# Performance work log

Hardware: AMD Instinct MI355X
Metric: run time of the kernel (lower is better)

## Reference

```python
import jax, jax.numpy as jnp
import numpy as np

B, FEAT, HID, LAT, NQ, NEMB = 2048, 840, 256, 128, 12, 512


def setup_inputs() -> dict:
    key = jax.random.key(0)
    ks = jax.random.split(key, 6)
    return {
        "x": jax.random.normal(ks[0], (B, FEAT), jnp.float32),
        "w1": jax.random.normal(ks[1], (HID, 1, 3), jnp.float32) * 0.1,   # Conv1d(1->256, k=3)
        "b1": jnp.zeros((HID,), jnp.float32),
        "w2": jax.random.normal(ks[2], (LAT, HID, 3), jnp.float32) * 0.05,  # Conv1d(256->128, k=3)
        "b2": jnp.zeros((LAT,), jnp.float32),
        # 12 codebooks of (512, 128), init uniform(-1/n_emb, 1/n_emb) per the torch code
        "codebooks": jax.random.uniform(ks[3], (NQ, NEMB, LAT), jnp.float32, -1.0 / NEMB, 1.0 / NEMB),
    }


def _encode(x, w1, b1, w2, b2):
    # x: (B, FEAT) -> unsqueeze channel dim -> NCW conv stack -> adaptive avg pool(1)
    h = x[:, None, :]  # (B, 1, FEAT)
    h = jax.lax.conv_general_dilated(h, w1, (1,), 'SAME',
                                     dimension_numbers=('NCH', 'OIH', 'NCH'))
    h = jax.nn.relu(h + b1[None, :, None])
    h = jax.lax.conv_general_dilated(h, w2, (1,), 'SAME',
                                     dimension_numbers=('NCH', 'OIH', 'NCH'))
    h = jax.nn.relu(h + b2[None, :, None])
    return h.mean(axis=2)  # AdaptiveAvgPool1d(1) + squeeze -> (B, LAT)


def _rvq(z_flat, codebooks):
    # sequential residual VQ: 12 stages of cdist -> argmin -> gather -> residual update
    def step(residual, cb):
        # squared L2 distances: ||r||^2 - 2 r C^T + ||c||^2, shape (B, NEMB)
        d = (jnp.sum(residual ** 2, axis=1, keepdims=True)
             - 2.0 * (residual @ cb.T)
             + jnp.sum(cb ** 2, axis=1)[None, :])
        idx = jnp.argmin(d, axis=1)          # (B,)
        q = cb[idx]                          # (B, LAT) embedding gather
        residual = residual - jax.lax.stop_gradient(q)  # .detach() in torch
        return residual, (q, idx)

    _, (qs, idxs) = jax.lax.scan(step, z_flat, codebooks)  # qs: (NQ, B, LAT)
    return qs.sum(axis=0), idxs.T  # (B, LAT), (B, NQ)


def reference(x, w1, b1, w2, b2, codebooks):
    z = _encode(x, w1, b1, w2, b2)            # (B, LAT)
    zq, idx = _rvq(z, codebooks)              # L = 1 so flat == (B, LAT)
    return zq[:, None, :], idx[:, None, :]    # (B, 1, LAT), (B, 1, NQ)
```

## Files before the change

kernel.cpp:

```cpp
#include <hip/hip_runtime.h>

#define B_SZ 2048
#define FEAT 840
#define HID  256
#define LAT  128
#define NQ   12
#define NEMB 512

#define T_SUB 40
#define NTILE 21
#define HSTR  46
#define H2STR 21
#define CQ    64
#define HBUF  (CQ * HSTR)

#define W2R_FLOATS ((size_t)HID * 384)
#define CBN_FLOATS ((size_t)NQ * NEMB)

__device__ __forceinline__ float np8_combine(const float* r) {
    float sA = __fadd_rn(r[0], r[1]);
    float sB = __fadd_rn(r[2], r[3]);
    float sC = __fadd_rn(r[4], r[5]);
    float sD = __fadd_rn(r[6], r[7]);
    return __fadd_rn(__fadd_rn(sA, sB), __fadd_rn(sC, sD));
}

__global__ __launch_bounds__(256) void w2r_kernel(const float* __restrict__ w2,
                                                  float* __restrict__ w2r)
{
    int p = blockIdx.x * 256 + threadIdx.x;
    if (p >= HID * 384) return;
    int c2 = p / 384, r = p - c2 * 384;
    int ly = r / 6, jk = r - ly * 6;
    int j = jk / 3, k = jk - j * 3;
    w2r[p] = w2[(size_t)(ly*2 + j)*768 + c2*3 + k];
}

__global__ __launch_bounds__(256) void cbn_kernel(const float* __restrict__ cb,
                                                  float* __restrict__ cbn)
{
    int p = blockIdx.x * 256 + threadIdx.x;
    if (p >= NQ * NEMB) return;
    const float* __restrict__ cp = cb + (size_t)p * LAT;
    float c8[8];
#pragma unroll
    for (int j = 0; j < 8; ++j) {
        float c = cp[j];
        c8[j] = __fmul_rn(c, c);
    }
    for (int i = 8; i < LAT; i += 8)
#pragma unroll
        for (int j = 0; j < 8; ++j) {
            float c = cp[i+j];
            c8[j] = __fadd_rn(c8[j], __fmul_rn(c, c));
        }
    cbn[p] = np8_combine(c8);
}

template <int USE_WR>
__global__ __launch_bounds__(256) void enc_kernel(
    const float* __restrict__ x,  const float* __restrict__ w1,
    const float* __restrict__ b1, const float* __restrict__ w2,
    const float* __restrict__ w2r,
    const float* __restrict__ b2, float* __restrict__ zout)
{
    __shared__ float xp[FEAT + 4];
    __shared__ float h1s[HBUF];
    __shared__ float leafs[LAT * 8];

    const int tid = threadIdx.x;
    const int b   = blockIdx.x;
    const int tx  = tid & 3;
    const int ly  = tid >> 2;
    const int u0  = tx * 10;

    const int ach   = tid >> 2;
    const int piece = tid & 3;
    const int tpb   = piece * 11;
    const int tpe   = (piece == 3) ? 42 : tpb + 11;

    float b2v[2];
    b2v[0] = b2[ly*2 + 0];
    b2v[1] = b2[ly*2 + 1];

    for (int i = tid; i < FEAT + 2; i += 256)
        xp[i] = (i >= 1 && i <= FEAT) ? x[(size_t)b*FEAT + i - 1] : 0.f;

    float racc[8];
    int leaf_id = 0, leaf_pos = 0;
#pragma unroll
    for (int j = 0; j < 8; ++j) racc[j] = 0.f;

    __syncthreads();
    for (int t0 = 0; t0 < FEAT; t0 += T_SUB) {
        const bool edge = (t0 == 0) | (t0 + T_SUB == FEAT);

        float sk[2][10][3];
#pragma unroll
        for (int j = 0; j < 2; ++j)
#pragma unroll
            for (int i = 0; i < 10; ++i)
#pragma unroll
                for (int k = 0; k < 3; ++k) sk[j][i][k] = 0.f;

#pragma unroll 1
        for (int qf = 0; qf < 4; ++qf) {
            {
                const int c = qf*CQ + ach;
                const float wA = w1[c*3+0], wB = w1[c*3+1], wC = w1[c*3+2];
                const float bb = b1[c];
                if (edge) {
                    for (int tp = tpb; tp < tpe; ++tp) {
                        int tg = t0 - 1 + tp;
                        float v = 0.f;
                        if (tg >= 0 && tg < FEAT) {
                            float s = __fadd_rn(__fadd_rn(__fmul_rn(wA, xp[tg]),
                                                          __fmul_rn(wB, xp[tg+1])),
                                                __fmul_rn(wC, xp[tg+2]));
                            s = __fadd_rn(s, bb);
                            v = s > 0.f ? s : 0.f;
                        }
                        h1s[ach*HSTR + tp] = v;
                    }
                } else {
#pragma unroll 11
                    for (int tp = tpb; tp < tpe; ++tp) {
                        int tg = t0 - 1 + tp;
                        float s = __fadd_rn(__fadd_rn(__fmul_rn(wA, xp[tg]),
                                                      __fmul_rn(wB, xp[tg+1])),
                                            __fmul_rn(wC, xp[tg+2]));
                        s = __fadd_rn(s, bb);
                        h1s[ach*HSTR + tp] = s > 0.f ? s : 0.f;
                    }
                }
            }
            __syncthreads();

            if (USE_WR) {
                const float* __restrict__ wbase =
                    w2r + (size_t)(qf*CQ)*384 + ly*6;
#pragma unroll 2
                for (int cc = 0; cc < CQ; ++cc) {
                    const float2* __restrict__ wq =
                        (const float2*)(wbase + (size_t)cc*384);
                    float2 W0 = wq[0], W1 = wq[1], W2 = wq[2];
                    float w_[6] = {W0.x, W0.y, W1.x, W1.y, W2.x, W2.y};

                    const float2* __restrict__ hq =
                        (const float2*)(&h1s[cc*HSTR + u0]);
                    float2 q0=hq[0], q1=hq[1], q2=hq[2], q3=hq[3], q4=hq[4], q5=hq[5];
                    float hv[12] = {q0.x,q0.y,q1.x,q1.y,q2.x,q2.y,
                                    q3.x,q3.y,q4.x,q4.y,q5.x,q5.y};
#pragma unroll
                    for (int j = 0; j < 2; ++j)
#pragma unroll
                        for (int i = 0; i < 10; ++i)
#pragma unroll
                            for (int k = 0; k < 3; ++k)
                                sk[j][i][k] = __fmaf_rn(w_[j*3+k], hv[i+k],
                                                        sk[j][i][k]);
                }
            } else {
                for (int cc = 0; cc < CQ; ++cc) {
                    int c2 = qf*CQ + cc;
                    const float* hp = &h1s[cc*HSTR + u0];
                    float hv[12];
#pragma unroll
                    for (int m = 0; m < 12; ++m) hv[m] = hp[m];
#pragma unroll
                    for (int j = 0; j < 2; ++j) {
                        float wa = w2[(size_t)(ly*2+j)*768 + c2*3 + 0];
                        float wb = w2[(size_t)(ly*2+j)*768 + c2*3 + 1];
                        float wc = w2[(size_t)(ly*2+j)*768 + c2*3 + 2];
#pragma unroll
                        for (int i = 0; i < 10; ++i) {
                            sk[j][i][0] = __fmaf_rn(wa, hv[i],   sk[j][i][0]);
                            sk[j][i][1] = __fmaf_rn(wb, hv[i+1], sk[j][i][1]);
                            sk[j][i][2] = __fmaf_rn(wc, hv[i+2], sk[j][i][2]);
                        }
                    }
                }
            }
            __syncthreads();
        }

#pragma unroll 1
        for (int st = 0; st < 2; ++st) {
            if ((tx >> 1) == st) {
#pragma unroll
                for (int j = 0; j < 2; ++j)
#pragma unroll
                    for (int i = 0; i < 10; ++i) {
                        float hh = __fadd_rn(__fadd_rn(sk[j][i][0], sk[j][i][1]),
                                             sk[j][i][2]);
                        hh = __fadd_rn(hh, b2v[j]);
                        hh = hh > 0.f ? hh : 0.f;
                        h1s[(ly*2 + j)*H2STR + (u0 - st*20) + i] = hh;
                    }
            }
            __syncthreads();

            if (tid < LAT) {
                for (int g = 0; g < 20; g += 10) {
                    float v[10];
#pragma unroll
                    for (int m = 0; m < 10; ++m)
                        v[m] = h1s[tid*H2STR + g + m];
#pragma unroll
                    for (int m = 0; m < 10; ++m) {
                        float vv = v[m];
                        int j = leaf_pos & 7;
                        racc[j] = (leaf_pos < 8) ? vv : __fadd_rn(racc[j], vv);
                        ++leaf_pos;
                        int llen = (leaf_id == 7) ? 112 : 104;
                        if (leaf_pos == llen) {
                            leafs[tid*8 + leaf_id] = np8_combine(racc);
                            ++leaf_id; leaf_pos = 0;
                        }
                    }
                }
            }
            __syncthreads();
        }
    }

    if (tid < LAT) {
        const float* L = &leafs[tid*8];
        float s0 = __fadd_rn(L[0], L[1]);
        float s1 = __fadd_rn(L[2], L[3]);
        float sA = __fadd_rn(s0, s1);
        float s2 = __fadd_rn(L[4], L[5]);
        float s3 = __fadd_rn(L[6], L[7]);
        float sB = __fadd_rn(s2, s3);
        float tot = __fadd_rn(sA, sB);
        zout[(size_t)b*LAT + tid] = __fdiv_rn(tot, 840.0f);
    }
}

template <int USE_CN>
__global__ __launch_bounds__(256) void rvq32_kernel(
    const float* __restrict__ cb, const float* __restrict__ cbn,
    const float* __restrict__ z,
    float* __restrict__ zqout, float* __restrict__ oidx)
{
    __shared__ float rr[LAT];
    __shared__ float Ash;
    __shared__ float redd[256];
    __shared__ int   rede[256];
    __shared__ float sredd[64];
    __shared__ int   srede[64];
    __shared__ int   beste;
    __shared__ float qv[NQ * LAT];

    const int tid = threadIdx.x;
    const int b   = blockIdx.x;

    if (tid < LAT) rr[tid] = z[(size_t)b*LAT + tid];
    __syncthreads();

    for (int q = 0; q < NQ; ++q) {
        const float* __restrict__ cbq = cb + (size_t)q * NEMB * LAT;

        if (tid == 0) {
            float r8[8];
#pragma unroll
            for (int j = 0; j < 8; ++j) r8[j] = __fmul_rn(rr[j], rr[j]);
            for (int i = 8; i < LAT; i += 8)
#pragma unroll
                for (int j = 0; j < 8; ++j)
                    r8[j] = __fadd_rn(r8[j], __fmul_rn(rr[i+j], rr[i+j]));
            Ash = np8_combine(r8);
        }
        __syncthreads();

        float dmin = 0.f; int emin = 0;
#pragma unroll
        for (int h = 0; h < 2; ++h) {
            int e = 2*tid + h;
            const float* __restrict__ cp = cbq + (size_t)e*LAT;
            float dot = 0.f;
            float cn;
            if (USE_CN) {
#pragma unroll
                for (int j = 0; j < 8; ++j)
                    dot = __fmaf_rn(cp[j], rr[j], dot);
                for (int i = 8; i < LAT; i += 8)
#pragma unroll
                    for (int j = 0; j < 8; ++j)
                        dot = __fmaf_rn(cp[i+j], rr[i+j], dot);
                cn = cbn[(size_t)q*NEMB + e];
            } else {
                float c8[8];
#pragma unroll
                for (int j = 0; j < 8; ++j) {
                    float c = cp[j];
                    c8[j] = __fmul_rn(c, c);
                    dot = __fmaf_rn(c, rr[j], dot);
                }
                for (int i = 8; i < LAT; i += 8)
#pragma unroll
                    for (int j = 0; j < 8; ++j) {
                        float c = cp[i+j];
                        dot = __fmaf_rn(c, rr[i+j], dot);
                        c8[j] = __fadd_rn(c8[j], __fmul_rn(c, c));
                    }
                cn = np8_combine(c8);
            }
            float G  = __fmul_rn(2.0f, dot);
            float d  = __fadd_rn(__fsub_rn(Ash, G), cn);
            if (h == 0) { dmin = d; emin = e; }
            else if (d < dmin) { dmin = d; emin = e; }
        }
        redd[tid] = dmin; rede[tid] = emin;
        __syncthreads();

        if (tid < 64) {
            float bb = redd[tid*4]; int ee = rede[tid*4];
            for (int j = 1; j < 4; ++j) {
                float dj = redd[tid*4 + j];
                if (dj < bb) { bb = dj; ee = rede[tid*4 + j]; }
            }
            sredd[tid] = bb; srede[tid] = ee;
        }
        __syncthreads();
        if (tid == 0) {
            float bb = sredd[0]; int ee = srede[0];
            for (int j = 1; j < 64; ++j) {
                float dj = sredd[j];
                if (dj < bb) { bb = dj; ee = srede[j]; }
            }
            beste = ee;
            oidx[(size_t)b*NQ + q] = (float)ee;
        }
        __syncthreads();

        if (tid < LAT) {
            float cv = cbq[(size_t)beste*LAT + tid];
            qv[q*LAT + tid] = cv;
            rr[tid] = __fsub_rn(rr[tid], cv);
        }
        __syncthreads();
    }

    if (tid < LAT) {
        float s = qv[tid];
        for (int s2 = 1; s2 < NQ; ++s2)
            s = __fadd_rn(s, qv[s2*LAT + tid]);
        zqout[(size_t)b*LAT + tid] = s;
    }
}

extern "C" void kernel_launch(void* const* d_in, const int* in_sizes, int n_in,
                              void* d_out, int out_size, void* d_ws, size_t ws_size,
                              hipStream_t stream)
{
    (void)in_sizes; (void)n_in; (void)out_size;
    const float* x  = (const float*)d_in[0];
    const float* w1 = (const float*)d_in[1];
    const float* b1 = (const float*)d_in[2];
    const float* w2 = (const float*)d_in[3];
    const float* b2 = (const float*)d_in[4];
    const float* cb = (const float*)d_in[5];

    float* out  = (float*)d_out;
    float* zq   = out;
    float* oidx = out + (size_t)B_SZ * LAT;

    const size_t w2r_bytes  = W2R_FLOATS * sizeof(float);
    const size_t full_bytes = (W2R_FLOATS + CBN_FLOATS) * sizeof(float);

    if (ws_size >= full_bytes) {
        float* w2r = (float*)d_ws;
        float* cbn = (float*)d_ws + W2R_FLOATS;
        w2r_kernel<<<(HID*384 + 255)/256, 256, 0, stream>>>(w2, w2r);
        cbn_kernel<<<(NQ*NEMB + 255)/256, 256, 0, stream>>>(cb, cbn);
        enc_kernel<1><<<B_SZ, 256, 0, stream>>>(x, w1, b1, w2, w2r, b2, zq);
        rvq32_kernel<1><<<B_SZ, 256, 0, stream>>>(cb, cbn, zq, zq, oidx);
    } else if (ws_size >= w2r_bytes) {
        float* w2r = (float*)d_ws;
        w2r_kernel<<<(HID*384 + 255)/256, 256, 0, stream>>>(w2, w2r);
        enc_kernel<1><<<B_SZ, 256, 0, stream>>>(x, w1, b1, w2, w2r, b2, zq);
        rvq32_kernel<0><<<B_SZ, 256, 0, stream>>>(cb, nullptr, zq, zq, oidx);
    } else {
        enc_kernel<0><<<B_SZ, 256, 0, stream>>>(x, w1, b1, w2, nullptr, b2, zq);
        rvq32_kernel<0><<<B_SZ, 256, 0, stream>>>(cb, nullptr, zq, zq, oidx);
    }
}
```

Before: 5.999 ms.

## Re-tile encoder conv to 60-step sub-tiles with 320 threads and transposed weights

The encoder block grows from 256 to 320 threads (5 groups of 64 output-channel pairs), and each thread now computes 12 time steps instead of 10. The time sub-tile grows from 40 to 60, cutting the outer tile count from 21 to 14 along with the syncs and h1 rebuilds tied to it. The reordered w2 layout puts the channel index innermost, so adjacent threads' weight loads coalesce instead of each thread reading its own float2 triplet. The costs are higher register pressure from 72 accumulators, a 5-step serialized write-out and reduction per tile, and a block size that may lower occupancy.

New measurement: 8.999 ms. 1.5x slower.

```diff
diff --git a/kernel.cpp b/kernel.cpp
--- a/kernel.cpp
+++ b/kernel.cpp
@@ -7,10 +7,10 @@
 #define NQ   12
 #define NEMB 512
 
-#define T_SUB 40
-#define NTILE 21
-#define HSTR  46
-#define H2STR 21
+#define T_SUB 60
+#define NTILE 14
+#define HSTR  62
+#define H2STR 13
 #define CQ    64
 #define HBUF  (CQ * HSTR)
 
@@ -26,14 +26,14 @@
 }
 
 __global__ __launch_bounds__(256) void w2r_kernel(const float* __restrict__ w2,
-                                                  float* __restrict__ w2r)
+                                                  float* __restrict__ w2t)
 {
     int p = blockIdx.x * 256 + threadIdx.x;
     if (p >= HID * 384) return;
     int c2 = p / 384, r = p - c2 * 384;
-    int ly = r / 6, jk = r - ly * 6;
-    int j = jk / 3, k = jk - j * 3;
-    w2r[p] = w2[(size_t)(ly*2 + j)*768 + c2*3 + k];
+    int m = r / 64, ly = r - m * 64;
+    int j = m / 3, k = m - j * 3;
+    w2t[p] = w2[(size_t)(2*ly + j)*768 + c2*3 + k];
 }
 
 __global__ __launch_bounds__(256) void cbn_kernel(const float* __restrict__ cb,
@@ -58,10 +58,10 @@
 }
 
 template <int USE_WR>
-__global__ __launch_bounds__(256) void enc_kernel(
+__global__ __launch_bounds__(320) void enc_kernel(
     const float* __restrict__ x,  const float* __restrict__ w1,
     const float* __restrict__ b1, const float* __restrict__ w2,
-    const float* __restrict__ w2r,
+    const float* __restrict__ w2t,
     const float* __restrict__ b2, float* __restrict__ zout)
 {
     __shared__ float xp[FEAT + 4];
@@ -70,20 +70,19 @@
 
     const int tid = threadIdx.x;
     const int b   = blockIdx.x;
-    const int tx  = tid & 3;
-    const int ly  = tid >> 2;
-    const int u0  = tx * 10;
-
-    const int ach   = tid >> 2;
-    const int piece = tid & 3;
-    const int tpb   = piece * 11;
-    const int tpe   = (piece == 3) ? 42 : tpb + 11;
+    const int ly  = tid & 63;
+    const int tx  = tid >> 6;
+    const int u0  = tx * 12;
+
+    const int ach = ly;
+    const int tpb = tx*12 + (tx < 2 ? tx : 2);
+    const int tpe = tpb + (tx < 2 ? 13 : 12);
 
     float b2v[2];
     b2v[0] = b2[ly*2 + 0];
     b2v[1] = b2[ly*2 + 1];
 
-    for (int i = tid; i < FEAT + 2; i += 256)
+    for (int i = tid; i < FEAT + 2; i += 320)
         xp[i] = (i >= 1 && i <= FEAT) ? x[(size_t)b*FEAT + i - 1] : 0.f;
 
     float racc[8];
@@ -95,11 +94,11 @@
     for (int t0 = 0; t0 < FEAT; t0 += T_SUB) {
         const bool edge = (t0 == 0) | (t0 + T_SUB == FEAT);
 
-        float sk[2][10][3];
+        float sk[2][12][3];
 #pragma unroll
         for (int j = 0; j < 2; ++j)
 #pragma unroll
-            for (int i = 0; i < 10; ++i)
+            for (int i = 0; i < 12; ++i)
 #pragma unroll
                 for (int k = 0; k < 3; ++k) sk[j][i][k] = 0.f;
 
@@ -123,7 +122,7 @@
                         h1s[ach*HSTR + tp] = v;
                     }
                 } else {
-#pragma unroll 11
+#pragma unroll
                     for (int tp = tpb; tp < tpe; ++tp) {
                         int tg = t0 - 1 + tp;
                         float s = __fadd_rn(__fadd_rn(__fmul_rn(wA, xp[tg]),
@@ -137,24 +136,27 @@
             __syncthreads();
 
             if (USE_WR) {
-                const float* __restrict__ wbase =
-                    w2r + (size_t)(qf*CQ)*384 + ly*6;
+                const float* __restrict__ wp =
+                    w2t + (size_t)(qf*CQ)*384 + ly;
 #pragma unroll 2
                 for (int cc = 0; cc < CQ; ++cc) {
-                    const float2* __restrict__ wq =
-                        (const float2*)(wbase + (size_t)cc*384);
-                    float2 W0 = wq[0], W1 = wq[1], W2 = wq[2];
-                    float w_[6] = {W0.x, W0.y, W1.x, W1.y, W2.x, W2.y};
+                    const float* __restrict__ wv = wp + (size_t)cc*384;
+                    float w_[6];
+#pragma unroll
+                    for (int m = 0; m < 6; ++m) w_[m] = wv[m*64];
 
                     const float2* __restrict__ hq =
                         (const float2*)(&h1s[cc*HSTR + u0]);
-                    float2 q0=hq[0], q1=hq[1], q2=hq[2], q3=hq[3], q4=hq[4], q5=hq[5];
-                    float hv[12] = {q0.x,q0.y,q1.x,q1.y,q2.x,q2.y,
-                                    q3.x,q3.y,q4.x,q4.y,q5.x,q5.y};
+                    float hv[14];
+#pragma unroll
+                    for (int m = 0; m < 7; ++m) {
+                        float2 q = hq[m];
+                        hv[2*m] = q.x; hv[2*m+1] = q.y;
+                    }
 #pragma unroll
                     for (int j = 0; j < 2; ++j)
 #pragma unroll
-                        for (int i = 0; i < 10; ++i)
+                        for (int i = 0; i < 12; ++i)
 #pragma unroll
                             for (int k = 0; k < 3; ++k)
                                 sk[j][i][k] = __fmaf_rn(w_[j*3+k], hv[i+k],
@@ -164,16 +166,16 @@
                 for (int cc = 0; cc < CQ; ++cc) {
                     int c2 = qf*CQ + cc;
                     const float* hp = &h1s[cc*HSTR + u0];
-                    float hv[12];
-#pragma unroll
-                    for (int m = 0; m < 12; ++m) hv[m] = hp[m];
+                    float hv[14];
+#pragma unroll
+                    for (int m = 0; m < 14; ++m) hv[m] = hp[m];
 #pragma unroll
                     for (int j = 0; j < 2; ++j) {
                         float wa = w2[(size_t)(ly*2+j)*768 + c2*3 + 0];
                         float wb = w2[(size_t)(ly*2+j)*768 + c2*3 + 1];
                         float wc = w2[(size_t)(ly*2+j)*768 + c2*3 + 2];
 #pragma unroll
-                        for (int i = 0; i < 10; ++i) {
+                        for (int i = 0; i < 12; ++i) {
                             sk[j][i][0] = __fmaf_rn(wa, hv[i],   sk[j][i][0]);
                             sk[j][i][1] = __fmaf_rn(wb, hv[i+1], sk[j][i][1]);
                             sk[j][i][2] = __fmaf_rn(wc, hv[i+2], sk[j][i][2]);
@@ -185,38 +187,36 @@
         }
 
 #pragma unroll 1
-        for (int st = 0; st < 2; ++st) {
-            if ((tx >> 1) == st) {
+        for (int st = 0; st < 5; ++st) {
+            if (tx == st) {
 #pragma unroll
                 for (int j = 0; j < 2; ++j)
 #pragma unroll
-                    for (int i = 0; i < 10; ++i) {
+                    for (int i = 0; i < 12; ++i) {
                         float hh = __fadd_rn(__fadd_rn(sk[j][i][0], sk[j][i][1]),
                                              sk[j][i][2]);
                         hh = __fadd_rn(hh, b2v[j]);
                         hh = hh > 0.f ? hh : 0.f;
-                        h1s[(ly*2 + j)*H2STR + (u0 - st*20) + i] = hh;
+                        h1s[(ly*2 + j)*H2STR + i] = hh;
                     }
             }
             __syncthreads();
 
             if (tid < LAT) {
-                for (int g = 0; g < 20; g += 10) {
-                    float v[10];
-#pragma unroll
-                    for (int m = 0; m < 10; ++m)
-                        v[m] = h1s[tid*H2STR + g + m];
-#pragma unroll
-                    for (int m = 0; m < 10; ++m) {
-                        float vv = v[m];
-                        int j = leaf_pos & 7;
-                        racc[j] = (leaf_pos < 8) ? vv : __fadd_rn(racc[j], vv);
-                        ++leaf_pos;
-                        int llen = (leaf_id == 7) ? 112 : 104;
-                        if (leaf_pos == llen) {
-                            leafs[tid*8 + leaf_id] = np8_combine(racc);
-                            ++leaf_id; leaf_pos = 0;
-                        }
+                float v[12];
+#pragma unroll
+                for (int m = 0; m < 12; ++m)
+                    v[m] = h1s[tid*H2STR + m];
+#pragma unroll
+                for (int m = 0; m < 12; ++m) {
+                    float vv = v[m];
+                    int j = leaf_pos & 7;
+                    racc[j] = (leaf_pos < 8) ? vv : __fadd_rn(racc[j], vv);
+                    ++leaf_pos;
+                    int llen = (leaf_id == 7) ? 112 : 104;
+                    if (leaf_pos == llen) {
+                        leafs[tid*8 + leaf_id] = np8_combine(racc);
+                        ++leaf_id; leaf_pos = 0;
                     }
                 }
             }
@@ -366,23 +366,23 @@
     float* zq   = out;
     float* oidx = out + (size_t)B_SZ * LAT;
 
-    const size_t w2r_bytes  = W2R_FLOATS * sizeof(float);
+    const size_t w2t_bytes  = W2R_FLOATS * sizeof(float);
     const size_t full_bytes = (W2R_FLOATS + CBN_FLOATS) * sizeof(float);
 
     if (ws_size >= full_bytes) {
-        float* w2r = (float*)d_ws;
+        float* w2t = (float*)d_ws;
         float* cbn = (float*)d_ws + W2R_FLOATS;
-        w2r_kernel<<<(HID*384 + 255)/256, 256, 0, stream>>>(w2, w2r);
+        w2r_kernel<<<(HID*384 + 255)/256, 256, 0, stream>>>(w2, w2t);
         cbn_kernel<<<(NQ*NEMB + 255)/256, 256, 0, stream>>>(cb, cbn);
-        enc_kernel<1><<<B_SZ, 256, 0, stream>>>(x, w1, b1, w2, w2r, b2, zq);
+        enc_kernel<1><<<B_SZ, 320, 0, stream>>>(x, w1, b1, w2, w2t, b2, zq);
         rvq32_kernel<1><<<B_SZ, 256, 0, stream>>>(cb, cbn, zq, zq, oidx);
-    } else if (ws_size >= w2r_bytes) {
-        float* w2r = (float*)d_ws;
-        w2r_kernel<<<(HID*384 + 255)/256, 256, 0, stream>>>(w2, w2r);
-        enc_kernel<1><<<B_SZ, 256, 0, stream>>>(x, w1, b1, w2, w2r, b2, zq);
+    } else if (ws_size >= w2t_bytes) {
+        float* w2t = (float*)d_ws;
+        w2r_kernel<<<(HID*384 + 255)/256, 256, 0, stream>>>(w2, w2t);
+        enc_kernel<1><<<B_SZ, 320, 0, stream>>>(x, w1, b1, w2, w2t, b2, zq);
         rvq32_kernel<0><<<B_SZ, 256, 0, stream>>>(cb, nullptr, zq, zq, oidx);
     } else {
-        enc_kernel<0><<<B_SZ, 256, 0, stream>>>(x, w1, b1, w2, nullptr, b2, zq);
+        enc_kernel<0><<<B_SZ, 320, 0, stream>>>(x, w1, b1, w2, nullptr, b2, zq);
         rvq32_kernel<0><<<B_SZ, 256, 0, stream>>>(cb, nullptr, zq, zq, oidx);
     }
 }
```
